# Performance work log

Hardware: AMD Instinct MI355X
Metric: run time of the kernel (lower is better)

Reference implementation:

```python
import jax, jax.numpy as jnp
import numpy as np

NUM_CHARTS = 16
LATENT_DIM = 128
RANK = 128
BATCH = 131072


def _init_weight(key, out_dim, in_dim):
    # nn.init.eye_ on top-left block, then += 0.01 * randn (identity-ish init)
    w = jnp.zeros((out_dim, in_dim), jnp.float32)
    m = min(out_dim, in_dim)
    w = w.at[jnp.arange(m), jnp.arange(m)].set(1.0)
    return w + 0.01 * jax.random.normal(key, (out_dim, in_dim), jnp.float32)


def setup_inputs() -> dict:
    key = jax.random.key(0)
    ks = jax.random.split(key, 3 + 2 * NUM_CHARTS)
    z_n = jax.random.normal(ks[0], (BATCH, LATENT_DIM), jnp.float32)
    source_idx = jax.random.randint(ks[1], (BATCH,), 0, NUM_CHARTS, dtype=jnp.int64 if jax.config.jax_enable_x64 else jnp.int32)
    target_idx = jax.random.randint(ks[2], (BATCH,), 0, NUM_CHARTS, dtype=source_idx.dtype)
    # encoder weights: [C, R, D] (torch Linear weight layout [out, in])
    enc_w = jnp.stack([_init_weight(ks[3 + i], RANK, LATENT_DIM) for i in range(NUM_CHARTS)])
    # decoder weights: [C, D, R]
    dec_w = jnp.stack([_init_weight(ks[3 + NUM_CHARTS + i], LATENT_DIM, RANK) for i in range(NUM_CHARTS)])
    c_param = jnp.zeros((NUM_CHARTS, RANK), jnp.float32)
    d_param = jnp.zeros((NUM_CHARTS, LATENT_DIM), jnp.float32)
    return {"z_n": z_n, "source_idx": source_idx, "target_idx": target_idx,
            "enc_w": enc_w, "dec_w": dec_w, "c_param": c_param, "d_param": d_param}


def _apply_per_chart(x, chart_idx, weights):
    # x: [B, in], weights: [C, out, in] -> [B, out]
    # Loop over the small fixed chart count; each chart does one dense GEMM,
    # results routed by mask-select (same math as gather/compute/scatter).
    C = weights.shape[0]
    out = jnp.zeros((x.shape[0], weights.shape[1]), x.dtype)
    for c in range(C):
        yc = x @ weights[c].T  # [B, out]
        out = jnp.where((chart_idx == c)[:, None], yc, out)
    return out


def reference(z_n, source_idx, target_idx, enc_w, dec_w, c_param, d_param):
    # lift_to_global: per-chart encode + bias c[src]
    h = _apply_per_chart(z_n, source_idx, enc_w) + c_param[source_idx]  # [B, R]
    # project_from_global: per-chart decode + bias d[tgt]
    z_out = _apply_per_chart(h, target_idx, dec_w) + d_param[target_idx]  # [B, D]
    return z_out
```

## Files before the change

kernel.cpp:

```cpp
#include <hip/hip_runtime.h>
#include <hip/hip_bf16.h>

#define NB     131072
#define NCH    16
#define NPAIR  256
#define LDW    136
#define LDH    136
#define LDO    132
#define CAP    1024

#define WS_HIST   0
#define WS_OFF    256
#define WS_SORTED 528
#define WS_BYTES  ((WS_SORTED + NB) * 4)

typedef short short8 __attribute__((ext_vector_type(8)));
typedef float f32x4  __attribute__((ext_vector_type(4)));

__device__ __forceinline__ short bfbits(float x) {
    union { __hip_bfloat16 h; short s; } u;
    u.h = __float2bfloat16(x);
    return u.s;
}

__device__ __forceinline__ short8 cvt_frag(const float* __restrict__ p) {
    const f32x4 lo = *(const f32x4*)p;
    const f32x4 hi = *(const f32x4*)(p + 4);
    short8 r;
    r[0] = bfbits(lo[0]); r[1] = bfbits(lo[1]); r[2] = bfbits(lo[2]); r[3] = bfbits(lo[3]);
    r[4] = bfbits(hi[0]); r[5] = bfbits(hi[1]); r[6] = bfbits(hi[2]); r[7] = bfbits(hi[3]);
    return r;
}

__device__ __forceinline__ short8 pack_frag(f32x4 lo, f32x4 hi) {
    short8 r;
    r[0] = bfbits(lo[0]); r[1] = bfbits(lo[1]); r[2] = bfbits(lo[2]); r[3] = bfbits(lo[3]);
    r[4] = bfbits(hi[0]); r[5] = bfbits(hi[1]); r[6] = bfbits(hi[2]); r[7] = bfbits(hi[3]);
    return r;
}

__global__ void k_init(int* __restrict__ hist) {
    hist[threadIdx.x] = 0;
}

__global__ __launch_bounds__(256) void k_hist(const int* __restrict__ si,
                                              const int* __restrict__ ti,
                                              int* __restrict__ hist) {
    __shared__ int sh[NPAIR];
    const int t = threadIdx.x;
    sh[t] = 0;
    __syncthreads();
    const int base = blockIdx.x * 1024 + t;
#pragma unroll
    for (int j = 0; j < 4; ++j) {
        const int i = base + j * 256;
        const int k = (si[i] * NCH + ti[i]) & (NPAIR - 1);
        atomicAdd(&sh[k], 1);
    }
    __syncthreads();
    if (sh[t]) atomicAdd(&hist[t], sh[t]);
}

__global__ __launch_bounds__(256) void k_scan(int* __restrict__ hist,
                                              int* __restrict__ off) {
    __shared__ int s[NPAIR];
    const int t = threadIdx.x;
    const int v = hist[t];
    s[t] = v;
    __syncthreads();
#pragma unroll
    for (int d = 1; d < NPAIR; d <<= 1) {
        const int x = (t >= d) ? s[t - d] : 0;
        __syncthreads();
        s[t] += x;
        __syncthreads();
    }
    off[t + 1] = s[t];
    if (t == 0) off[0] = 0;
    hist[t] = s[t] - v;
}

__global__ __launch_bounds__(256) void k_scatter(const int* __restrict__ si,
                                                 const int* __restrict__ ti,
                                                 int* __restrict__ cursor,
                                                 int* __restrict__ sorted) {
    __shared__ int sh[NPAIR];
    __shared__ int sbase[NPAIR];
    const int t = threadIdx.x;
    sh[t] = 0;
    __syncthreads();
    int key[4], rank[4];
    const int base = blockIdx.x * 1024 + t;
#pragma unroll
    for (int j = 0; j < 4; ++j) {
        const int i = base + j * 256;
        const int k = (si[i] * NCH + ti[i]) & (NPAIR - 1);
        key[j]  = k;
        rank[j] = atomicAdd(&sh[k], 1);
    }
    __syncthreads();
    sbase[t] = sh[t] ? atomicAdd(&cursor[t], sh[t]) : 0;
    __syncthreads();
#pragma unroll
    for (int j = 0; j < 4; ++j) {
        const int slot = sbase[key[j]] + rank[j];
        if (slot >= 0 && slot < NB)
            sorted[slot] = base + j * 256;
    }
}

__global__ __launch_bounds__(512, 2)
void k_gemm(const float* __restrict__ z,
            const float* __restrict__ encw,
            const float* __restrict__ decw,
            const float* __restrict__ cpar,
            const float* __restrict__ dpar,
            const int* __restrict__ off,
            const int* __restrict__ sorted,
            float* __restrict__ out) {
    __shared__ int sRowLds[CAP];
    __shared__ __align__(16) __hip_bfloat16 sW1[128 * LDW];
    __shared__ __align__(16) __hip_bfloat16 sW2[128 * LDW];
    __shared__ __align__(16) __hip_bfloat16 sH[8 * 32 * LDH];

    const int bucket = blockIdx.x;
    const int srcc = bucket >> 4;
    const int tgtc = bucket & (NCH - 1);
    const int beg = off[bucket];
    const int end = off[bucket + 1];

    const int tid  = threadIdx.x;
    const int lane = tid & 63;
    const int wv   = tid >> 6;
    const int lr   = lane & 15;
    const int lhi  = lane >> 4;

    {
        const float* W1 = encw + srcc * 16384;
        const float* W2 = decw + tgtc * 16384;
#pragma unroll
        for (int it = 0; it < 4; ++it) {
            const int f = (it * 512 + tid) * 8;
            const int row = f >> 7, col = f & 127;
            *(short8*)(sW1 + row * LDW + col) = cvt_frag(W1 + f);
            *(short8*)(sW2 + row * LDW + col) = cvt_frag(W2 + f);
        }
    }

    float cb[8], db[8];
#pragma unroll
    for (int nt = 0; nt < 8; ++nt) {
        cb[nt] = cpar[srcc * 128 + nt * 16 + lr];
        db[nt] = dpar[tgtc * 128 + nt * 16 + lr];
    }

    __hip_bfloat16* const hs = sH + wv * (32 * LDH);

    f32x4 bufA[8], bufB[8];

    auto pf = [&](int g) {
        const int r0 = sRowLds[(g << 5) + lr];
        const int r1 = sRowLds[(g << 5) + 16 + lr];
        const float* p0 = z + (long)(r0 < 0 ? 0 : r0) * 128 + lhi * 8;
        const float* p1 = z + (long)(r1 < 0 ? 0 : r1) * 128 + lhi * 8;
#pragma unroll
        for (int k = 0; k < 4; ++k) {
            bufA[2 * k]     = *(const f32x4*)(p0 + k * 32);
            bufA[2 * k + 1] = *(const f32x4*)(p0 + k * 32 + 4);
            bufB[2 * k]     = *(const f32x4*)(p1 + k * 32);
            bufB[2 * k + 1] = *(const f32x4*)(p1 + k * 32 + 4);
        }
    };

    for (int cb0 = beg; cb0 < end; cb0 += CAP) {
        const int cnt = min(end - cb0, CAP);
        __syncthreads();
        for (int i = tid; i < CAP; i += 512) {
            int v = (i < cnt) ? sorted[cb0 + i] : -1;
            sRowLds[i] = ((unsigned)v < (unsigned)NB) ? v : -1;
        }
        __syncthreads();

        const int ng = (cnt + 31) >> 5;
        int g = wv;
        if (g < ng) pf(g);
        while (g < ng) {
            short8 a0[4], a1[4];
#pragma unroll
            for (int k = 0; k < 4; ++k) {
                a0[k] = pack_frag(bufA[2 * k], bufA[2 * k + 1]);
                a1[k] = pack_frag(bufB[2 * k], bufB[2 * k + 1]);
            }
            const int gn = g + 8;
            if (gn < ng) pf(gn);

            f32x4 acc0[8], acc1[8];
#pragma unroll
            for (int nt = 0; nt < 8; ++nt) { acc0[nt] = (f32x4)(0.0f); acc1[nt] = (f32x4)(0.0f); }

#pragma unroll
            for (int k = 0; k < 4; ++k) {
#pragma unroll
                for (int nt = 0; nt < 8; ++nt) {
                    const short8 b = *(const short8*)(sW1 + (nt * 16 + lr) * LDW + k * 32 + lhi * 8);
                    acc0[nt] = __builtin_amdgcn_mfma_f32_16x16x32_bf16(a0[k], b, acc0[nt], 0, 0, 0);
                    acc1[nt] = __builtin_amdgcn_mfma_f32_16x16x32_bf16(a1[k], b, acc1[nt], 0, 0, 0);
                }
            }

#pragma unroll
            for (int nt = 0; nt < 8; ++nt)
#pragma unroll
                for (int r = 0; r < 4; ++r) {
                    hs[(lhi * 4 + r) * LDH + nt * 16 + lr]        = __float2bfloat16(acc0[nt][r] + cb[nt]);
                    hs[(16 + lhi * 4 + r) * LDH + nt * 16 + lr]   = __float2bfloat16(acc1[nt][r] + cb[nt]);
                }

#pragma unroll
            for (int nt = 0; nt < 8; ++nt) { acc0[nt] = (f32x4)(0.0f); acc1[nt] = (f32x4)(0.0f); }

#pragma unroll
            for (int k = 0; k < 4; ++k) {
                const short8 ah0 = *(const short8*)(hs + lr * LDH + k * 32 + lhi * 8);
                const short8 ah1 = *(const short8*)(hs + (16 + lr) * LDH + k * 32 + lhi * 8);
#pragma unroll
                for (int nt = 0; nt < 8; ++nt) {
                    const short8 b = *(const short8*)(sW2 + (nt * 16 + lr) * LDW + k * 32 + lhi * 8);
                    acc0[nt] = __builtin_amdgcn_mfma_f32_16x16x32_bf16(ah0, b, acc0[nt], 0, 0, 0);
                    acc1[nt] = __builtin_amdgcn_mfma_f32_16x16x32_bf16(ah1, b, acc1[nt], 0, 0, 0);
                }
            }

            {
                int g0[4], g1[4];
#pragma unroll
                for (int r = 0; r < 4; ++r) {
                    g0[r] = sRowLds[(g << 5) + lhi * 4 + r];
                    g1[r] = sRowLds[(g << 5) + 16 + lhi * 4 + r];
                }
#pragma unroll
                for (int nt = 0; nt < 8; ++nt)
#pragma unroll
                    for (int r = 0; r < 4; ++r) {
                        if (g0[r] >= 0)
                            out[(long)g0[r] * 128 + nt * 16 + lr] = acc0[nt][r] + db[nt];
                        if (g1[r] >= 0)
                            out[(long)g1[r] * 128 + nt * 16 + lr] = acc1[nt][r] + db[nt];
                    }
            }
            g = gn;
        }
    }
}

__global__ __launch_bounds__(256)
void k_fallback(const float* __restrict__ z,
                const int* __restrict__ si, const int* __restrict__ ti,
                const float* __restrict__ ew,
                const float* __restrict__ dw,
                const float* __restrict__ cp,
                const float* __restrict__ dp,
                float* __restrict__ out) {
    __shared__ float sh[4][128];
    const int lane = threadIdx.x & 63, wv = threadIdx.x >> 6;
    for (int row = blockIdx.x * 4 + wv; row < NB; row += (int)gridDim.x * 4) {
        const int sc = si[row] & (NCH - 1), tc = ti[row] & (NCH - 1);
        const float* zr = z + (long)row * 128;
        const float* W1 = ew + sc * 16384;
        float h0 = cp[sc * 128 + lane];
        float h1 = cp[sc * 128 + lane + 64];
        for (int d = 0; d < 128; ++d) {
            const float zv = zr[d];
            h0 += zv * W1[lane * 128 + d];
            h1 += zv * W1[(lane + 64) * 128 + d];
        }
        sh[wv][lane] = h0;
        sh[wv][lane + 64] = h1;
        __syncthreads();
        const float* W2 = dw + tc * 16384;
        float o0 = dp[tc * 128 + lane];
        float o1 = dp[tc * 128 + lane + 64];
        for (int r = 0; r < 128; ++r) {
            const float hv = sh[wv][r];
            o0 += hv * W2[lane * 128 + r];
            o1 += hv * W2[(lane + 64) * 128 + r];
        }
        out[(long)row * 128 + lane] = o0;
        out[(long)row * 128 + lane + 64] = o1;
        __syncthreads();
    }
}

extern "C" void kernel_launch(void* const* d_in, const int* in_sizes, int n_in,
                              void* d_out, int out_size, void* d_ws, size_t ws_size,
                              hipStream_t stream) {
    const float* z  = (const float*)d_in[0];
    const int*   si = (const int*)d_in[1];
    const int*   ti = (const int*)d_in[2];
    const float* ew = (const float*)d_in[3];
    const float* dw = (const float*)d_in[4];
    const float* cp = (const float*)d_in[5];
    const float* dp = (const float*)d_in[6];
    float* out = (float*)d_out;

    if (ws_size >= (size_t)WS_BYTES) {
        int* hist   = (int*)d_ws + WS_HIST;
        int* off    = (int*)d_ws + WS_OFF;
        int* sorted = (int*)d_ws + WS_SORTED;

        k_init<<<1, NPAIR, 0, stream>>>(hist);
        k_hist<<<128, 256, 0, stream>>>(si, ti, hist);
        k_scan<<<1, NPAIR, 0, stream>>>(hist, off);
        k_scatter<<<128, 256, 0, stream>>>(si, ti, hist, sorted);
        k_gemm<<<NPAIR, 512, 0, stream>>>(z, ew, dw, cp, dp, off, sorted, out);
    } else {
        k_fallback<<<1024, 256, 0, stream>>>(z, si, ti, ew, dw, cp, dp, out);
    }
}
```

Measured before the change: 145.4 us.

## Pre-convert weights to swizzled bf16 and use a new 256-thread GEMM kernel

Merges the histogram pass with a one-time fp32-to-bf16 conversion of the encoder and decoder weights into workspace, stored in XOR-swizzled layout. A new GEMM kernel loads these with direct global-to-LDS loads, runs two blocks per chart pair with 16-row groups per wave, and software-prefetches the next z rows. Results are written straight to global memory without an LDS staging pass. The memset replaces the init kernel. The new path needs a larger workspace and adds a conversion pass, and each wave now handles fewer rows per iteration.

After: 164.5 us. 1.13x slower.

```diff
diff --git a/kernel.cpp b/kernel.cpp
--- a/kernel.cpp
+++ b/kernel.cpp
@@ -6,13 +6,14 @@
 #define NPAIR  256
 #define LDW    136
 #define LDH    136
-#define LDO    132
 #define CAP    1024
 
 #define WS_HIST   0
 #define WS_OFF    256
 #define WS_SORTED 528
+#define WS_WBF    131600
 #define WS_BYTES  ((WS_SORTED + NB) * 4)
+#define WS_FULL   (WS_BYTES + 2 * 16 * 16384 * 2)
 
 typedef short short8 __attribute__((ext_vector_type(8)));
 typedef float f32x4  __attribute__((ext_vector_type(4)));
@@ -39,26 +40,47 @@
     return r;
 }
 
-__global__ void k_init(int* __restrict__ hist) {
-    hist[threadIdx.x] = 0;
-}
-
-__global__ __launch_bounds__(256) void k_hist(const int* __restrict__ si,
-                                              const int* __restrict__ ti,
-                                              int* __restrict__ hist) {
+__device__ __forceinline__ void gload_lds16(const void* g, void* l) {
+    __builtin_amdgcn_global_load_lds(
+        (const __attribute__((address_space(1))) void*)g,
+        (__attribute__((address_space(3))) void*)l, 16, 0, 0);
+}
+
+__global__ __launch_bounds__(256) void k_pre(const int* __restrict__ si,
+                                             const int* __restrict__ ti,
+                                             int* __restrict__ hist,
+                                             const float* __restrict__ encw,
+                                             const float* __restrict__ decw,
+                                             short* __restrict__ wbf) {
     __shared__ int sh[NPAIR];
+    const int bid = blockIdx.x;
     const int t = threadIdx.x;
-    sh[t] = 0;
-    __syncthreads();
-    const int base = blockIdx.x * 1024 + t;
-#pragma unroll
-    for (int j = 0; j < 4; ++j) {
-        const int i = base + j * 256;
-        const int k = (si[i] * NCH + ti[i]) & (NPAIR - 1);
-        atomicAdd(&sh[k], 1);
-    }
-    __syncthreads();
-    if (sh[t]) atomicAdd(&hist[t], sh[t]);
+    if (bid < 128) {
+        sh[t] = 0;
+        __syncthreads();
+        const int base = bid * 1024 + t;
+#pragma unroll
+        for (int j = 0; j < 4; ++j) {
+            const int i = base + j * 256;
+            const int k = (si[i] * NCH + ti[i]) & (NPAIR - 1);
+            atomicAdd(&sh[k], 1);
+        }
+        __syncthreads();
+        if (sh[t]) atomicAdd(&hist[t], sh[t]);
+    } else {
+#pragma unroll
+        for (int j = 0; j < 4; ++j) {
+            const int G   = (bid - 128) * 1024 + j * 256 + t;
+            const int gi  = G & 15;
+            const int row = (G >> 4) & 127;
+            const int ch  = (G >> 11) & 15;
+            const int mat = G >> 15;
+            const float* src = (mat ? decw : encw) + ch * 16384 + row * 128
+                             + ((gi ^ (row & 7)) << 3);
+            short* dst = wbf + mat * 262144 + ch * 16384 + row * 128 + (gi << 3);
+            *(short8*)dst = cvt_frag(src);
+        }
+    }
 }
 
 __global__ __launch_bounds__(256) void k_scan(int* __restrict__ hist,
@@ -107,6 +129,164 @@
         if (slot >= 0 && slot < NB)
             sorted[slot] = base + j * 256;
     }
+}
+
+__global__ __launch_bounds__(256, 2)
+void k_gemm2(const float* __restrict__ z,
+             const short* __restrict__ wbf,
+             const float* __restrict__ cpar,
+             const float* __restrict__ dpar,
+             const int* __restrict__ off,
+             const int* __restrict__ sorted,
+             float* __restrict__ out) {
+    __shared__ __align__(16) short sW1[16384];
+    __shared__ __align__(16) short sW2[16384];
+    __shared__ __align__(16) short sH[4 * 2048];
+
+    const int bucket = blockIdx.x >> 1;
+    const int half   = blockIdx.x & 1;
+    const int srcc = bucket >> 4;
+    const int tgtc = bucket & (NCH - 1);
+    const int beg = off[bucket];
+    const int end = off[bucket + 1];
+
+    const int tid  = threadIdx.x;
+    const int lane = tid & 63;
+    const int wv   = tid >> 6;
+    const int lr   = lane & 15;
+    const int lhi  = lane >> 4;
+    const int swz  = (lr & 7) << 3;
+
+    {
+        const short* w1 = wbf + srcc * 16384;
+        const short* w2 = wbf + 262144 + tgtc * 16384;
+#pragma unroll
+        for (int i = 0; i < 8; ++i) {
+            const int o = (wv * 8 + i) * 512;
+            gload_lds16(w1 + o + lane * 8, sW1 + o);
+            gload_lds16(w2 + o + lane * 8, sW2 + o);
+        }
+    }
+
+    float cb[8], db[8];
+#pragma unroll
+    for (int nt = 0; nt < 8; ++nt) {
+        cb[nt] = cpar[srcc * 128 + nt * 16 + lr];
+        db[nt] = dpar[tgtc * 128 + nt * 16 + lr];
+    }
+
+    short* const hs = sH + wv * 2048;
+    const int slot = half * 4 + wv;
+    const int ng   = (end - beg + 15) >> 4;
+
+    f32x4 buf[8];
+    int g = slot;
+    int rIdx = -1;
+    if (g < ng) {
+        const int idx = beg + (g << 4) + lr;
+        int v = (idx < end) ? sorted[idx] : -1;
+        rIdx = ((unsigned)v < (unsigned)NB) ? v : -1;
+        const float* p = z + (long)(rIdx < 0 ? 0 : rIdx) * 128 + lhi * 8;
+#pragma unroll
+        for (int k = 0; k < 4; ++k) {
+            buf[2 * k]     = *(const f32x4*)(p + k * 32);
+            buf[2 * k + 1] = *(const f32x4*)(p + k * 32 + 4);
+        }
+    }
+    __syncthreads();
+
+    while (g < ng) {
+        short8 a[4];
+#pragma unroll
+        for (int k = 0; k < 4; ++k) a[k] = pack_frag(buf[2 * k], buf[2 * k + 1]);
+        const int rCur = rIdx;
+        const int gn = g + 8;
+        int rN = -1;
+        if (gn < ng) {
+            const int idx = beg + (gn << 4) + lr;
+            int v = (idx < end) ? sorted[idx] : -1;
+            rN = ((unsigned)v < (unsigned)NB) ? v : -1;
+        }
+
+        f32x4 acc[8];
+#pragma unroll
+        for (int nt = 0; nt < 8; ++nt) acc[nt] = (f32x4)(0.0f);
+#pragma unroll
+        for (int k = 0; k < 4; ++k) {
+            const int kc = k * 32 + lhi * 8;
+#pragma unroll
+            for (int nt = 0; nt < 8; ++nt) {
+                const short8 b = *(const short8*)(sW1 + (nt * 16 + lr) * 128 + (kc ^ swz));
+                acc[nt] = __builtin_amdgcn_mfma_f32_16x16x32_bf16(a[k], b, acc[nt], 0, 0, 0);
+            }
+        }
+
+        if (gn < ng) {
+            const float* p = z + (long)(rN < 0 ? 0 : rN) * 128 + lhi * 8;
+#pragma unroll
+            for (int k = 0; k < 4; ++k) {
+                buf[2 * k]     = *(const f32x4*)(p + k * 32);
+                buf[2 * k + 1] = *(const f32x4*)(p + k * 32 + 4);
+            }
+        }
+
+#pragma unroll
+        for (int nt = 0; nt < 8; ++nt)
+#pragma unroll
+            for (int r = 0; r < 4; ++r) {
+                const int row = lhi * 4 + r;
+                hs[row * 128 + ((nt * 16 + lr) ^ ((row & 7) << 3))] =
+                    bfbits(acc[nt][r] + cb[nt]);
+            }
+
+#pragma unroll
+        for (int nt = 0; nt < 8; ++nt) acc[nt] = (f32x4)(0.0f);
+#pragma unroll
+        for (int k = 0; k < 4; ++k) {
+            const int kc = k * 32 + lhi * 8;
+            const short8 ah = *(const short8*)(hs + lr * 128 + (kc ^ swz));
+#pragma unroll
+            for (int nt = 0; nt < 8; ++nt) {
+                const short8 b = *(const short8*)(sW2 + (nt * 16 + lr) * 128 + (kc ^ swz));
+                acc[nt] = __builtin_amdgcn_mfma_f32_16x16x32_bf16(ah, b, acc[nt], 0, 0, 0);
+            }
+        }
+
+        int grow[4];
+#pragma unroll
+        for (int r = 0; r < 4; ++r) grow[r] = __shfl(rCur, lhi * 4 + r, 16);
+#pragma unroll
+        for (int nt = 0; nt < 8; ++nt)
+#pragma unroll
+            for (int r = 0; r < 4; ++r)
+                if (grow[r] >= 0)
+                    out[(long)grow[r] * 128 + nt * 16 + lr] = acc[nt][r] + db[nt];
+
+        rIdx = rN;
+        g = gn;
+    }
+}
+
+__global__ void k_init(int* __restrict__ hist) {
+    hist[threadIdx.x] = 0;
+}
+
+__global__ __launch_bounds__(256) void k_hist(const int* __restrict__ si,
+                                              const int* __restrict__ ti,
+                                              int* __restrict__ hist) {
+    __shared__ int sh[NPAIR];
+    const int t = threadIdx.x;
+    sh[t] = 0;
+    __syncthreads();
+    const int base = blockIdx.x * 1024 + t;
+#pragma unroll
+    for (int j = 0; j < 4; ++j) {
+        const int i = base + j * 256;
+        const int k = (si[i] * NCH + ti[i]) & (NPAIR - 1);
+        atomicAdd(&sh[k], 1);
+    }
+    __syncthreads();
+    if (sh[t]) atomicAdd(&hist[t], sh[t]);
 }
 
 __global__ __launch_bounds__(512, 2)
@@ -155,7 +335,6 @@
     }
 
     __hip_bfloat16* const hs = sH + wv * (32 * LDH);
-
     f32x4 bufA[8], bufB[8];
 
     auto pf = [&](int g) {
@@ -212,8 +391,8 @@
             for (int nt = 0; nt < 8; ++nt)
 #pragma unroll
                 for (int r = 0; r < 4; ++r) {
-                    hs[(lhi * 4 + r) * LDH + nt * 16 + lr]        = __float2bfloat16(acc0[nt][r] + cb[nt]);
-                    hs[(16 + lhi * 4 + r) * LDH + nt * 16 + lr]   = __float2bfloat16(acc1[nt][r] + cb[nt]);
+                    hs[(lhi * 4 + r) * LDH + nt * 16 + lr]      = __float2bfloat16(acc0[nt][r] + cb[nt]);
+                    hs[(16 + lhi * 4 + r) * LDH + nt * 16 + lr] = __float2bfloat16(acc1[nt][r] + cb[nt]);
                 }
 
 #pragma unroll
@@ -303,7 +482,18 @@
     const float* dp = (const float*)d_in[6];
     float* out = (float*)d_out;
 
-    if (ws_size >= (size_t)WS_BYTES) {
+    if (ws_size >= (size_t)WS_FULL) {
+        int*   hist   = (int*)d_ws + WS_HIST;
+        int*   off    = (int*)d_ws + WS_OFF;
+        int*   sorted = (int*)d_ws + WS_SORTED;
+        short* wbf    = (short*)((int*)d_ws + WS_WBF);
+
+        (void)hipMemsetAsync(hist, 0, NPAIR * sizeof(int), stream);
+        k_pre<<<192, 256, 0, stream>>>(si, ti, hist, ew, dw, wbf);
+        k_scan<<<1, NPAIR, 0, stream>>>(hist, off);
+        k_scatter<<<128, 256, 0, stream>>>(si, ti, hist, sorted);
+        k_gemm2<<<512, 256, 0, stream>>>(z, wbf, cp, dp, off, sorted, out);
+    } else if (ws_size >= (size_t)WS_BYTES) {
         int* hist   = (int*)d_ws + WS_HIST;
         int* off    = (int*)d_ws + WS_OFF;
         int* sorted = (int*)d_ws + WS_SORTED;
```

## Fuse histogram, scan and scatter into one cooperative kernel with grid sync

Applied to the files above, without the earlier changes.

Replaces the four small sort-stage launches (init, hist, scan, scatter) with a memset and one cooperative kernel. A grid-wide sync separates the histogram from a per-block redundant scan and the scatter. The aim is to remove launch gaps and serialization between the tiny kernels. In exchange it adds cooperative-launch overhead and a grid barrier, and keeps the old path as a fallback if the cooperative launch fails.

New measurement: 174.9 us. 1.2x slower.

```diff
diff --git a/kernel.cpp b/kernel.cpp
--- a/kernel.cpp
+++ b/kernel.cpp
@@ -1,17 +1,20 @@
 #include <hip/hip_runtime.h>
 #include <hip/hip_bf16.h>
+#include <hip/hip_cooperative_groups.h>
+
+namespace cg = cooperative_groups;
 
 #define NB     131072
 #define NCH    16
 #define NPAIR  256
 #define LDW    136
 #define LDH    136
-#define LDO    132
 #define CAP    1024
 
 #define WS_HIST   0
-#define WS_OFF    256
-#define WS_SORTED 528
+#define WS_BCUR   256
+#define WS_OFF    512
+#define WS_SORTED 769
 #define WS_BYTES  ((WS_SORTED + NB) * 4)
 
 typedef short short8 __attribute__((ext_vector_type(8)));
@@ -39,58 +42,20 @@
     return r;
 }
 
-__global__ void k_init(int* __restrict__ hist) {
-    hist[threadIdx.x] = 0;
-}
-
-__global__ __launch_bounds__(256) void k_hist(const int* __restrict__ si,
-                                              const int* __restrict__ ti,
-                                              int* __restrict__ hist) {
+__global__ __launch_bounds__(256)
+void k_sort(const int* __restrict__ si, const int* __restrict__ ti,
+            int* __restrict__ hist, int* __restrict__ bcur,
+            int* __restrict__ off, int* __restrict__ sorted) {
     __shared__ int sh[NPAIR];
-    const int t = threadIdx.x;
+    __shared__ int sc[NPAIR];
+    __shared__ int sbase[NPAIR];
+    cg::grid_group grid = cg::this_grid();
+    const int t = threadIdx.x, bid = blockIdx.x;
+
     sh[t] = 0;
     __syncthreads();
-    const int base = blockIdx.x * 1024 + t;
-#pragma unroll
-    for (int j = 0; j < 4; ++j) {
-        const int i = base + j * 256;
-        const int k = (si[i] * NCH + ti[i]) & (NPAIR - 1);
-        atomicAdd(&sh[k], 1);
-    }
-    __syncthreads();
-    if (sh[t]) atomicAdd(&hist[t], sh[t]);
-}
-
-__global__ __launch_bounds__(256) void k_scan(int* __restrict__ hist,
-                                              int* __restrict__ off) {
-    __shared__ int s[NPAIR];
-    const int t = threadIdx.x;
-    const int v = hist[t];
-    s[t] = v;
-    __syncthreads();
-#pragma unroll
-    for (int d = 1; d < NPAIR; d <<= 1) {
-        const int x = (t >= d) ? s[t - d] : 0;
-        __syncthreads();
-        s[t] += x;
-        __syncthreads();
-    }
-    off[t + 1] = s[t];
-    if (t == 0) off[0] = 0;
-    hist[t] = s[t] - v;
-}
-
-__global__ __launch_bounds__(256) void k_scatter(const int* __restrict__ si,
-                                                 const int* __restrict__ ti,
-                                                 int* __restrict__ cursor,
-                                                 int* __restrict__ sorted) {
-    __shared__ int sh[NPAIR];
-    __shared__ int sbase[NPAIR];
-    const int t = threadIdx.x;
-    sh[t] = 0;
-    __syncthreads();
     int key[4], rank[4];
-    const int base = blockIdx.x * 1024 + t;
+    const int base = bid * 1024 + t;
 #pragma unroll
     for (int j = 0; j < 4; ++j) {
         const int i = base + j * 256;
@@ -99,7 +64,26 @@
         rank[j] = atomicAdd(&sh[k], 1);
     }
     __syncthreads();
-    sbase[t] = sh[t] ? atomicAdd(&cursor[t], sh[t]) : 0;
+    const int cnt = sh[t];
+    if (cnt) atomicAdd(&hist[t], cnt);
+    grid.sync();
+
+    const int v = __hip_atomic_load(&hist[t], __ATOMIC_RELAXED, __HIP_MEMORY_SCOPE_AGENT);
+    sc[t] = v;
+    __syncthreads();
+#pragma unroll
+    for (int d = 1; d < NPAIR; d <<= 1) {
+        const int x = (t >= d) ? sc[t - d] : 0;
+        __syncthreads();
+        sc[t] += x;
+        __syncthreads();
+    }
+    if (bid == 0) {
+        off[t + 1] = sc[t];
+        if (t == 0) off[0] = 0;
+    }
+    const int excl = sc[t] - v;
+    sbase[t] = cnt ? (excl + atomicAdd(&bcur[t], cnt)) : 0;
     __syncthreads();
 #pragma unroll
     for (int j = 0; j < 4; ++j) {
@@ -155,7 +139,6 @@
     }
 
     __hip_bfloat16* const hs = sH + wv * (32 * LDH);
-
     f32x4 bufA[8], bufB[8];
 
     auto pf = [&](int g) {
@@ -212,8 +195,8 @@
             for (int nt = 0; nt < 8; ++nt)
 #pragma unroll
                 for (int r = 0; r < 4; ++r) {
-                    hs[(lhi * 4 + r) * LDH + nt * 16 + lr]        = __float2bfloat16(acc0[nt][r] + cb[nt]);
-                    hs[(16 + lhi * 4 + r) * LDH + nt * 16 + lr]   = __float2bfloat16(acc1[nt][r] + cb[nt]);
+                    hs[(lhi * 4 + r) * LDH + nt * 16 + lr]      = __float2bfloat16(acc0[nt][r] + cb[nt]);
+                    hs[(16 + lhi * 4 + r) * LDH + nt * 16 + lr] = __float2bfloat16(acc1[nt][r] + cb[nt]);
                 }
 
 #pragma unroll
@@ -250,6 +233,76 @@
             }
             g = gn;
         }
+    }
+}
+
+__global__ void k_init(int* __restrict__ hist) {
+    hist[threadIdx.x] = 0;
+}
+
+__global__ __launch_bounds__(256) void k_hist(const int* __restrict__ si,
+                                              const int* __restrict__ ti,
+                                              int* __restrict__ hist) {
+    __shared__ int sh[NPAIR];
+    const int t = threadIdx.x;
+    sh[t] = 0;
+    __syncthreads();
+    const int base = blockIdx.x * 1024 + t;
+#pragma unroll
+    for (int j = 0; j < 4; ++j) {
+        const int i = base + j * 256;
+        const int k = (si[i] * NCH + ti[i]) & (NPAIR - 1);
+        atomicAdd(&sh[k], 1);
+    }
+    __syncthreads();
+    if (sh[t]) atomicAdd(&hist[t], sh[t]);
+}
+
+__global__ __launch_bounds__(256) void k_scan(int* __restrict__ hist,
+                                              int* __restrict__ off) {
+    __shared__ int s[NPAIR];
+    const int t = threadIdx.x;
+    const int v = hist[t];
+    s[t] = v;
+    __syncthreads();
+#pragma unroll
+    for (int d = 1; d < NPAIR; d <<= 1) {
+        const int x = (t >= d) ? s[t - d] : 0;
+        __syncthreads();
+        s[t] += x;
+        __syncthreads();
+    }
+    off[t + 1] = s[t];
+    if (t == 0) off[0] = 0;
+    hist[t] = s[t] - v;
+}
+
+__global__ __launch_bounds__(256) void k_scatter(const int* __restrict__ si,
+                                                 const int* __restrict__ ti,
+                                                 int* __restrict__ cursor,
+                                                 int* __restrict__ sorted) {
+    __shared__ int sh[NPAIR];
+    __shared__ int sbase[NPAIR];
+    const int t = threadIdx.x;
+    sh[t] = 0;
+    __syncthreads();
+    int key[4], rank[4];
+    const int base = blockIdx.x * 1024 + t;
+#pragma unroll
+    for (int j = 0; j < 4; ++j) {
+        const int i = base + j * 256;
+        const int k = (si[i] * NCH + ti[i]) & (NPAIR - 1);
+        key[j]  = k;
+        rank[j] = atomicAdd(&sh[k], 1);
+    }
+    __syncthreads();
+    sbase[t] = sh[t] ? atomicAdd(&cursor[t], sh[t]) : 0;
+    __syncthreads();
+#pragma unroll
+    for (int j = 0; j < 4; ++j) {
+        const int slot = sbase[key[j]] + rank[j];
+        if (slot >= 0 && slot < NB)
+            sorted[slot] = base + j * 256;
     }
 }
 
@@ -305,13 +358,35 @@
 
     if (ws_size >= (size_t)WS_BYTES) {
         int* hist   = (int*)d_ws + WS_HIST;
+        int* bcur   = (int*)d_ws + WS_BCUR;
         int* off    = (int*)d_ws + WS_OFF;
         int* sorted = (int*)d_ws + WS_SORTED;
 
-        k_init<<<1, NPAIR, 0, stream>>>(hist);
-        k_hist<<<128, 256, 0, stream>>>(si, ti, hist);
-        k_scan<<<1, NPAIR, 0, stream>>>(hist, off);
-        k_scatter<<<128, 256, 0, stream>>>(si, ti, hist, sorted);
+        static int coopChecked = 0, coopOK = 0;
+        if (!coopChecked) {
+            coopChecked = 1;
+            int dev = 0;
+            (void)hipGetDevice(&dev);
+            (void)hipDeviceGetAttribute(&coopOK, hipDeviceAttributeCooperativeLaunch, dev);
+        }
+
+        bool sorted_ok = false;
+        if (coopOK) {
+            (void)hipMemsetAsync(hist, 0, 2 * NPAIR * sizeof(int), stream);
+            void* args[] = { (void*)&si, (void*)&ti, (void*)&hist,
+                             (void*)&bcur, (void*)&off, (void*)&sorted };
+            hipError_t e = hipLaunchCooperativeKernel((const void*)k_sort,
+                                                      dim3(128), dim3(256),
+                                                      args, 0, stream);
+            if (e == hipSuccess) sorted_ok = true;
+            else (void)hipGetLastError();
+        }
+        if (!sorted_ok) {
+            k_init<<<1, NPAIR, 0, stream>>>(hist);
+            k_hist<<<128, 256, 0, stream>>>(si, ti, hist);
+            k_scan<<<1, NPAIR, 0, stream>>>(hist, off);
+            k_scatter<<<128, 256, 0, stream>>>(si, ti, hist, sorted);
+        }
         k_gemm<<<NPAIR, 512, 0, stream>>>(z, ew, dw, cp, dp, off, sorted, out);
     } else {
         k_fallback<<<1024, 256, 0, stream>>>(z, si, ti, ew, dw, cp, dp, out);
```
